# Kernel optimization log

Measured on AMD Instinct MI355X. Metric: run time of the kernel, lower is better.

Reference implementation:

```python
import jax, jax.numpy as jnp
import numpy as np

B, S, D = 2, 2048, 1024
H, KV, HD = 16, 4, 64
F, E, K = 2816, 8, 2
EPS = 1e-6

def setup_inputs() -> dict:
    key = jax.random.key(0)
    ks = jax.random.split(key, 9)
    def rn(k, shape, std=0.02):
        return jax.random.normal(k, shape, dtype=jnp.float32) * std
    inv_freq = 1.0 / (10000.0 ** (jnp.arange(0, HD, 2, dtype=jnp.float32) / HD))
    freqs = jnp.arange(S, dtype=jnp.float32)[:, None] * inv_freq[None, :]
    emb = jnp.concatenate([freqs, freqs], axis=-1)  # [S, HD]
    return {
        'hidden_states': rn(ks[0], (B, S, D), 1.0),
        'ln1_w': jnp.ones((D,), jnp.float32),
        'ln2_w': jnp.ones((D,), jnp.float32),
        'q_w': rn(ks[1], (H * HD, D)), 'q_b': jnp.zeros((H * HD,), jnp.float32),
        'k_w': rn(ks[2], (KV * HD, D)), 'k_b': jnp.zeros((KV * HD,), jnp.float32),
        'v_w': rn(ks[3], (KV * HD, D)), 'v_b': jnp.zeros((KV * HD,), jnp.float32),
        'o_w': rn(ks[4], (D, H * HD)),
        'router_w': rn(ks[5], (E, D), 0.01),
        'gate_w': rn(ks[6], (E, D, F)),
        'up_w': rn(ks[7], (E, D, F)),
        'down_w': rn(ks[8], (E, F, D)),
        'cos': jnp.cos(emb), 'sin': jnp.sin(emb),
    }

def _rmsnorm(x, w):
    v = jnp.mean(jnp.square(x.astype(jnp.float32)), axis=-1, keepdims=True)
    return (x.astype(jnp.float32) * jax.lax.rsqrt(v + EPS)).astype(x.dtype) * w

def _rotate_half(x):
    h = x.shape[-1] // 2
    return jnp.concatenate([-x[..., h:], x[..., :h]], axis=-1)

def reference(hidden_states, ln1_w, ln2_w, q_w, q_b, k_w, k_b, v_w, v_b, o_w, router_w, gate_w, up_w, down_w, cos, sin):
    # --- attention block (RMSNorm -> Qwen2Attention with RoPE+GQA -> residual) ---
    residual = hidden_states
    h = _rmsnorm(hidden_states, ln1_w)
    q = (h @ q_w.T + q_b).reshape(B, S, H, HD).transpose(0, 2, 1, 3)   # [B,H,S,HD]
    k = (h @ k_w.T + k_b).reshape(B, S, KV, HD).transpose(0, 2, 1, 3)  # [B,KV,S,HD]
    v = (h @ v_w.T + v_b).reshape(B, S, KV, HD).transpose(0, 2, 1, 3)
    c = cos[None, None]; s = sin[None, None]
    q = q * c + _rotate_half(q) * s
    k = k * c + _rotate_half(k) * s
    rep = H // KV
    k = jnp.repeat(k, rep, axis=1)
    v = jnp.repeat(v, rep, axis=1)
    scores = jnp.einsum('bhqd,bhkd->bhqk', q, k) / jnp.sqrt(jnp.float32(HD))
    causal = jnp.tril(jnp.ones((S, S), dtype=bool))
    scores = jnp.where(causal[None, None], scores, jnp.finfo(scores.dtype).min)
    attn = jax.nn.softmax(scores, axis=-1)
    ctx = jnp.einsum('bhqk,bhkd->bhqd', attn, v).transpose(0, 2, 1, 3).reshape(B, S, H * HD)
    x = ctx @ o_w.T + residual
    # --- MoE block (RMSNorm -> router -> expert SwiGLU MLPs -> combine -> residual) ---
    residual = x
    t = _rmsnorm(x, ln2_w).reshape(-1, D)  # [T, D], T = B*S
    logits = t @ router_w.T                # [T, E]
    probs = jax.nn.softmax(logits, axis=-1)
    topk_p, topk_i = jax.lax.top_k(probs, K)
    topk_p = topk_p / jnp.sum(topk_p, axis=-1, keepdims=True)
    # dispatch/combine weights [T,E]: vectorized form of the per-token scatter loop
    w = jnp.sum(jax.nn.one_hot(topk_i, E, dtype=t.dtype) * topk_p[..., None], axis=1)
    aux_loss = jnp.mean(E * jnp.square(jnp.mean(probs, axis=0)))
    out = jnp.zeros_like(t)
    for e in range(E):  # fixed small expert loop
        he = jax.nn.silu(t @ gate_w[e]) * (t @ up_w[e])
        out = out + (he @ down_w[e]) * w[:, e:e + 1]
    x = out.reshape(B, S, D) + residual
    return (x, aux_loss)
```

## Files before the change

kernel.cpp:

```cpp
#include <hip/hip_runtime.h>
#include <hip/hip_bf16.h>

#define DEVI __device__ __forceinline__

typedef float f32x4 __attribute__((ext_vector_type(4)));
typedef _Float16 f16x8 __attribute__((ext_vector_type(8)));
typedef short s16x8 __attribute__((ext_vector_type(8)));
typedef unsigned int u32;

constexpr int Bc = 2, Sc = 2048, Dc = 1024, Hc = 16, KVc = 4, HDc = 64, Fc = 2816, Ec = 8;
constexpr int Tc = Bc * Sc;
constexpr int QKVN = Hc * HDc + 2 * KVc * HDc;
constexpr int CAP = Tc * 2 + Ec * 128;
constexpr float LO_SCALE = 1024.0f;
constexpr float LO_INV = 1.0f / 1024.0f;

DEVI f32x4 mfma16(f16x8 a, f16x8 b, f32x4 c) {
    return __builtin_amdgcn_mfma_f32_16x16x32_f16(a, b, c, 0, 0, 0);
}
DEVI f32x4 mfma16(s16x8 a, s16x8 b, f32x4 c) {
    return __builtin_amdgcn_mfma_f32_16x16x32_bf16(a, b, c, 0, 0, 0);
}

DEVI void gll16(const void *g, void *l) {
    __builtin_amdgcn_global_load_lds(
        (const __attribute__((address_space(1))) u32 *)g,
        (__attribute__((address_space(3))) u32 *)l, 16, 0, 0);
}

DEVI u32 pack2(_Float16 a, _Float16 b) {
    union { _Float16 h[2]; u32 u; } t;
    t.h[0] = a; t.h[1] = b;
    return t.u;
}

template <int N> DEVI void wait_vm() {
    if constexpr (N == 0) asm volatile("s_waitcnt vmcnt(0)" ::: "memory");
    else if constexpr (N == 3) asm volatile("s_waitcnt vmcnt(3)" ::: "memory");
    else if constexpr (N == 4) asm volatile("s_waitcnt vmcnt(4)" ::: "memory");
    else if constexpr (N == 6) asm volatile("s_waitcnt vmcnt(6)" ::: "memory");
    else if constexpr (N == 8) asm volatile("s_waitcnt vmcnt(8)" ::: "memory");
}

template <typename VT> struct FragT;
template <> struct FragT<_Float16> { using type = f16x8; };
template <> struct FragT<__hip_bfloat16> { using type = s16x8; };

struct GemmP {
    const void *Ah, *Al;
    const void *Bh, *Bl, *Bh2;
    long lda, ldb, bExp, K;
    const int *poff, *gidx;
    const float *bias, *resid, *bw;
    float *outF, *outF2;
    __hip_bfloat16 *outBF;
    long ldc;
    int epi;
};

template <typename VT, bool SPLIT, bool GATHER, bool GU, int BN>
__global__ __launch_bounds__(256, SPLIT ? 3 : ((GU && BN == 128) ? 2 : 4)) void gemm_k(GemmP p) {
    constexpr int BM = 128;
    constexpr int NJ = BN / 32;
    constexpr bool HAS2 = SPLIT || GU;
    constexpr int ACH = SPLIT ? 1024 : 512;
    constexpr int BCH = BN * 4;
    constexpr int NB = HAS2 ? 2 : 1;
    constexpr int TOT = ACH + NB * BCH;
    constexpr int NCH = TOT / 256;
    constexpr int BUFVT = TOT * 8;
    constexpr int AOFF2 = 4096;
    constexpr int BOFF = ACH * 8;
    constexpr int B2OFF = (ACH + BCH) * 8;
    __shared__ __align__(16) VT s[2][BUFVT];
    const int tid = threadIdx.x, lane = tid & 63;
    const int wid = tid >> 6, wm = wid >> 1, wn = wid & 1;
    const int x = lane & 15, hi = lane >> 4;
    long m0 = (long)blockIdx.x * BM, n0 = (long)blockIdx.y * BN;
    int e = 0;
    if (p.poff) {
        int tot = p.poff[Ec];
        if (m0 >= tot) return;
        while (m0 >= p.poff[e + 1]) ++e;
    }

    const VT *gs[NCH];
    int chd[NCH];
#pragma unroll
    for (int i = 0; i < NCH; ++i) {
        int ch = tid + i * 256;
        chd[i] = ch;
        if (ch < ACH) {
            int slab = ch >> 9, local = ch & 511;
            int r = local >> 2, c = local & 3;
            int cs = c ^ ((r >> 1) & 3);
            long ar = m0 + r;
            if (GATHER) ar = p.gidx[ar];
            const VT *mat = (SPLIT && slab == 1) ? (const VT *)p.Al : (const VT *)p.Ah;
            gs[i] = mat + ar * p.lda + cs * 8;
        } else {
            int idx = ch - ACH;
            int which = idx / BCH, local = idx % BCH;
            int r = local >> 2, c = local & 3;
            int cs = c ^ ((r >> 1) & 3);
            const VT *bmat = (which == 0) ? (const VT *)p.Bh
                           : (SPLIT ? (const VT *)p.Bl : (const VT *)p.Bh2);
            gs[i] = bmat + (long)e * p.bExp + (n0 + r) * p.ldb + cs * 8;
        }
    }

    f32x4 acc[4][NJ];
    f32x4 acc2[HAS2 ? 4 : 1][HAS2 ? NJ : 1];
#pragma unroll
    for (int i = 0; i < 4; ++i)
#pragma unroll
        for (int j = 0; j < NJ; ++j) {
            acc[i][j] = (f32x4){0.f, 0.f, 0.f, 0.f};
            if constexpr (HAS2) acc2[i][j] = (f32x4){0.f, 0.f, 0.f, 0.f};
        }

    using F8 = typename FragT<VT>::type;
    const int KT = (int)(p.K / 32);
    auto stageTo = [&](int kt, int b) {
#pragma unroll
        for (int i = 0; i < NCH; ++i)
            gll16(gs[i] + (long)kt * 32, &s[b][(size_t)chd[i] * 8]);
    };

    stageTo(0, 0);
    if (KT > 1) stageTo(1, 1);

    for (int kt = 0; kt < KT; ++kt) {
        if (kt + 1 < KT) wait_vm<NCH>();
        else wait_vm<0>();
        __builtin_amdgcn_sched_barrier(0);
        __builtin_amdgcn_s_barrier();
        __builtin_amdgcn_sched_barrier(0);
        const int cur = kt & 1;

        F8 afh[4], afl[SPLIT ? 4 : 1];
#pragma unroll
        for (int mi = 0; mi < 4; ++mi) {
            int ar = wm * 64 + mi * 16 + x;
            int ad = (ar * 4 + (hi ^ ((ar >> 1) & 3))) * 8;
            afh[mi] = *(const F8 *)&s[cur][ad];
            if constexpr (SPLIT) afl[mi] = *(const F8 *)&s[cur][AOFF2 + ad];
        }
        __builtin_amdgcn_s_setprio(1);
#pragma unroll
        for (int nj = 0; nj < NJ; ++nj) {
            int br = wn * (BN / 2) + nj * 16 + x;
            int bd = (br * 4 + (hi ^ ((br >> 1) & 3))) * 8;
            F8 bfh = *(const F8 *)&s[cur][BOFF + bd];
            F8 bf2;
            if constexpr (HAS2) bf2 = *(const F8 *)&s[cur][B2OFF + bd];
#pragma unroll
            for (int mi = 0; mi < 4; ++mi) {
                acc[mi][nj] = mfma16(afh[mi], bfh, acc[mi][nj]);
                if constexpr (SPLIT) {
                    acc2[mi][nj] = mfma16(afh[mi], bf2, acc2[mi][nj]);
                    acc2[mi][nj] = mfma16(afl[mi], bfh, acc2[mi][nj]);
                }
                if constexpr (GU) acc2[mi][nj] = mfma16(afh[mi], bf2, acc2[mi][nj]);
            }
        }
        __builtin_amdgcn_s_setprio(0);

        asm volatile("s_waitcnt lgkmcnt(0)" ::: "memory");
        __builtin_amdgcn_sched_barrier(0);
        __builtin_amdgcn_s_barrier();
        __builtin_amdgcn_sched_barrier(0);
        if (kt + 2 < KT) stageTo(kt + 2, cur);
    }

#pragma unroll
    for (int mi = 0; mi < 4; ++mi)
#pragma unroll
        for (int nj = 0; nj < NJ; ++nj)
#pragma unroll
            for (int r = 0; r < 4; ++r) {
                long row = m0 + wm * 64 + mi * 16 + hi * 4 + r;
                long col = n0 + wn * (BN / 2) + nj * 16 + x;
                float v = acc[mi][nj][r];
                if constexpr (GU) {
                    float u = acc2[mi][nj][r];
                    float he = v / (1.f + __expf(-v)) * u;
                    p.outBF[row * p.ldc + col] = __float2bfloat16(he);
                } else {
                    if constexpr (SPLIT) v = fmaf(acc2[mi][nj][r], LO_INV, v);
                    switch (p.epi) {
                    case 0: p.outF[row * p.ldc + col] = v + p.bias[col]; break;
                    case 2: {
                        float o = v + p.resid[row * p.ldc + col];
                        p.outF[row * p.ldc + col] = o;
                        p.outF2[row * p.ldc + col] = o;
                    } break;
                    case 5: {
                        float wv = p.bw[row];
                        atomicAdd(&p.outF[(long)p.gidx[row] * p.ldc + col], v * wv);
                    } break;
                    }
                }
            }
}

__global__ __launch_bounds__(128, 2) void attn_k(
    const _Float16 *__restrict__ qh, const _Float16 *__restrict__ ql,
    const _Float16 *__restrict__ kh, const _Float16 *__restrict__ kl,
    const _Float16 *__restrict__ vTh, const _Float16 *__restrict__ vTl,
    _Float16 *__restrict__ ctxh, _Float16 *__restrict__ ctxl) {
    __shared__ __align__(16) _Float16 kbuf[2][2][32 * 64];
    __shared__ __align__(16) _Float16 vbuf[2][2][64 * 32];
    const int tid = threadIdx.x, lane = tid & 63, wid = tid >> 6;
    const int x = lane & 15, hi = lane >> 4;
    const int pairI = blockIdx.x;
    const int bh = blockIdx.y;
    const int b = bh >> 4, h = bh & 15, kvh = h >> 2;
    const long kRow0 = (long)b * Sc * 256;
    const long vRow0 = (long)(b * 4 + kvh) * 64 * (long)Sc;

    auto stage = [&](int kt, int bufI) {
        if (wid == 0) {
#pragma unroll
            for (int ss = 0; ss < 2; ++ss) {
                const _Float16 *src = ss ? kl : kh;
#pragma unroll
                for (int i = 0; i < 4; ++i) {
                    int kv = 8 * i + (lane >> 3);
                    int cd = (lane & 7) ^ (kv & 7);
                    const _Float16 *g = src + kRow0 + ((long)kt * 32 + kv) * 256 + kvh * 64 + cd * 8;
                    gll16(g, &kbuf[bufI][ss][i * 512]);
                }
            }
        } else {
#pragma unroll
            for (int ss = 0; ss < 2; ++ss) {
                const _Float16 *src = ss ? vTl : vTh;
#pragma unroll
                for (int i = 0; i < 4; ++i) {
                    int d = 16 * i + (lane >> 2);
                    int ckv = (lane & 3) ^ ((d >> 1) & 3);
                    const _Float16 *g = src + vRow0 + (long)d * Sc + (long)kt * 32 + ckv * 8;
                    gll16(g, &vbuf[bufI][ss][i * 512]);
                }
            }
        }
    };

    for (int seg = 0; seg < 2; ++seg) {
        const int qt = seg ? (63 - pairI) : pairI;
        const int q0 = qt * 32;
        const long qtokW = (long)b * Sc + q0 + wid * 16;

        f16x8 qfh[2], qfl[2];
#pragma unroll
        for (int ks = 0; ks < 2; ++ks) {
            long off = (qtokW + x) * (long)Dc + h * 64 + ks * 32 + hi * 8;
            qfh[ks] = *(const f16x8 *)(qh + off);
            qfl[ks] = *(const f16x8 *)(ql + off);
        }
        asm volatile("s_waitcnt vmcnt(0)" ::: "memory");
        __builtin_amdgcn_sched_barrier(0);

        f32x4 o1[4], o2[4];
        float mrow = -3.0e38f, lrow = 0.f;
#pragma unroll
        for (int dj = 0; dj < 4; ++dj) {
            o1[dj] = (f32x4){0.f, 0.f, 0.f, 0.f};
            o2[dj] = (f32x4){0.f, 0.f, 0.f, 0.f};
        }

        const int NT = qt + 1;

        stage(0, 0);
        stage(1, 1);

        for (int kt = 0; kt < NT; ++kt) {
            if (kt + 1 < NT) asm volatile("s_waitcnt vmcnt(8)" ::: "memory");
            else asm volatile("s_waitcnt vmcnt(0)" ::: "memory");
            __builtin_amdgcn_sched_barrier(0);
            __builtin_amdgcn_s_barrier();
            __builtin_amdgcn_sched_barrier(0);
            const int cur = kt & 1;

            f32x4 s1[2], s2[2];
#pragma unroll
            for (int kvs = 0; kvs < 2; ++kvs) {
                s1[kvs] = (f32x4){0.f, 0.f, 0.f, 0.f};
                s2[kvs] = (f32x4){0.f, 0.f, 0.f, 0.f};
            }
            __builtin_amdgcn_s_setprio(1);
#pragma unroll
            for (int ks = 0; ks < 2; ++ks)
#pragma unroll
                for (int kvs = 0; kvs < 2; ++kvs) {
                    int row = kvs * 16 + x;
                    int addr = row * 64 + (((ks * 4 + hi) ^ (row & 7)) << 3);
                    f16x8 kfh = *(const f16x8 *)&kbuf[cur][0][addr];
                    f16x8 kfl = *(const f16x8 *)&kbuf[cur][1][addr];
                    s1[kvs] = mfma16(kfh, qfh[ks], s1[kvs]);
                    s2[kvs] = mfma16(kfl, qfh[ks], s2[kvs]);
                    s2[kvs] = mfma16(kfh, qfl[ks], s2[kvs]);
                }
            __builtin_amdgcn_s_setprio(0);

            const bool diag = (kt == NT - 1);
            const int qpos = q0 + wid * 16 + x;
            float sv[2][4];
#pragma unroll
            for (int kvs = 0; kvs < 2; ++kvs)
#pragma unroll
                for (int r = 0; r < 4; ++r) {
                    float v = fmaf(s2[kvs][r], LO_INV, s1[kvs][r]) * 0.125f;
                    if (diag) {
                        int kvpos = kt * 32 + kvs * 16 + 4 * hi + r;
                        if (kvpos > qpos) v = -3.0e38f;
                    }
                    sv[kvs][r] = v;
                }
            float mx = sv[0][0];
#pragma unroll
            for (int kvs = 0; kvs < 2; ++kvs)
#pragma unroll
                for (int r = 0; r < 4; ++r) mx = fmaxf(mx, sv[kvs][r]);
            mx = fmaxf(mx, __shfl_xor(mx, 16));
            mx = fmaxf(mx, __shfl_xor(mx, 32));
            if (!__all(mx - mrow <= 8.0f)) {
                float mnew = fmaxf(mrow, mx);
                float scl = __expf(mrow - mnew);
                mrow = mnew;
                lrow *= scl;
                float sclr[4];
#pragma unroll
                for (int r = 0; r < 4; ++r) sclr[r] = __shfl(scl, 4 * hi + r);
#pragma unroll
                for (int dj = 0; dj < 4; ++dj)
#pragma unroll
                    for (int r = 0; r < 4; ++r) {
                        o1[dj][r] *= sclr[r];
                        o2[dj][r] *= sclr[r];
                    }
            }
            float pv[2][4];
            float ls = 0.f;
#pragma unroll
            for (int kvs = 0; kvs < 2; ++kvs)
#pragma unroll
                for (int r = 0; r < 4; ++r) {
                    pv[kvs][r] = __expf(sv[kvs][r] - mrow);
                    ls += pv[kvs][r];
                }
            ls += __shfl_xor(ls, 16);
            ls += __shfl_xor(ls, 32);
            lrow += ls;
            u32 Bh0[2], Bh1[2], Bl0[2], Bl1[2];
#pragma unroll
            for (int pr = 0; pr < 2; ++pr) {
                _Float16 a0 = (_Float16)pv[0][2 * pr], a1 = (_Float16)pv[0][2 * pr + 1];
                _Float16 b0 = (_Float16)pv[1][2 * pr], b1 = (_Float16)pv[1][2 * pr + 1];
                Bh0[pr] = pack2(a0, a1);
                Bh1[pr] = pack2(b0, b1);
                _Float16 la0 = (_Float16)((pv[0][2 * pr] - (float)a0) * LO_SCALE);
                _Float16 la1 = (_Float16)((pv[0][2 * pr + 1] - (float)a1) * LO_SCALE);
                _Float16 lb0 = (_Float16)((pv[1][2 * pr] - (float)b0) * LO_SCALE);
                _Float16 lb1 = (_Float16)((pv[1][2 * pr + 1] - (float)b1) * LO_SCALE);
                Bl0[pr] = pack2(la0, la1);
                Bl1[pr] = pack2(lb0, lb1);
            }
            const int srcLow = x + ((lane & 16) ? 32 : 0);
            const int srcHigh = srcLow + 16;
            const bool useB1 = lane >= 32;
            union { u32 u[4]; f16x8 v; } fh, fl;
#pragma unroll
            for (int pr = 0; pr < 2; ++pr) {
                u32 t0 = (u32)__shfl((int)Bh0[pr], srcLow);
                u32 t1 = (u32)__shfl((int)Bh1[pr], srcLow);
                fh.u[pr] = useB1 ? t1 : t0;
                u32 u0 = (u32)__shfl((int)Bh0[pr], srcHigh);
                u32 u1 = (u32)__shfl((int)Bh1[pr], srcHigh);
                fh.u[2 + pr] = useB1 ? u1 : u0;
                u32 s0 = (u32)__shfl((int)Bl0[pr], srcLow);
                u32 s1v = (u32)__shfl((int)Bl1[pr], srcLow);
                fl.u[pr] = useB1 ? s1v : s0;
                u32 w0 = (u32)__shfl((int)Bl0[pr], srcHigh);
                u32 w1 = (u32)__shfl((int)Bl1[pr], srcHigh);
                fl.u[2 + pr] = useB1 ? w1 : w0;
            }
            f16x8 pah = fh.v, pal = fl.v;

            __builtin_amdgcn_s_setprio(1);
#pragma unroll
            for (int dj = 0; dj < 4; ++dj) {
                int d = dj * 16 + x;
                int addr = d * 32 + ((hi ^ ((d >> 1) & 3)) << 3);
                f16x8 vhf = *(const f16x8 *)&vbuf[cur][0][addr];
                f16x8 vlf = *(const f16x8 *)&vbuf[cur][1][addr];
                o1[dj] = mfma16(pah, vhf, o1[dj]);
                o2[dj] = mfma16(pah, vlf, o2[dj]);
                o2[dj] = mfma16(pal, vhf, o2[dj]);
            }
            __builtin_amdgcn_s_setprio(0);

            asm volatile("s_waitcnt lgkmcnt(0)" ::: "memory");
            __builtin_amdgcn_sched_barrier(0);
            __builtin_amdgcn_s_barrier();
            __builtin_amdgcn_sched_barrier(0);
            if (kt + 2 < NT) stage(kt + 2, cur);
        }

        float linv = 1.0f / lrow;
        float lr[4];
#pragma unroll
        for (int r = 0; r < 4; ++r) lr[r] = __shfl(linv, 4 * hi + r);
#pragma unroll
        for (int dj = 0; dj < 4; ++dj)
#pragma unroll
            for (int r = 0; r < 4; ++r) {
                long tok = qtokW + 4 * hi + r;
                float ov = fmaf(o2[dj][r], LO_INV, o1[dj][r]) * lr[r];
                _Float16 hv = (_Float16)ov;
                long off = tok * Dc + h * 64 + dj * 16 + x;
                ctxh[off] = hv;
                ctxl[off] = (_Float16)((ov - (float)hv) * LO_SCALE);
            }
    }
}

__global__ __launch_bounds__(256) void rmsnorm_split_k(const float *__restrict__ x,
        const float *__restrict__ w, _Float16 *__restrict__ oh, _Float16 *__restrict__ ol) {
    const long row = blockIdx.x;
    const int tid = threadIdx.x, lane = tid & 63, wid = tid >> 6;
    f32x4 v = *(const f32x4 *)(x + row * Dc + tid * 4);
    float ss = v[0] * v[0] + v[1] * v[1] + v[2] * v[2] + v[3] * v[3];
#pragma unroll
    for (int off = 1; off < 64; off <<= 1) ss += __shfl_xor(ss, off);
    __shared__ float sw[4];
    if (lane == 0) sw[wid] = ss;
    __syncthreads();
    float inv = 1.0f / sqrtf((sw[0] + sw[1] + sw[2] + sw[3]) * (1.f / Dc) + 1e-6f);
#pragma unroll
    for (int j = 0; j < 4; ++j) {
        float y = v[j] * inv * w[tid * 4 + j];
        _Float16 hv = (_Float16)y;
        oh[row * Dc + tid * 4 + j] = hv;
        ol[row * Dc + tid * 4 + j] = (_Float16)((y - (float)hv) * LO_SCALE);
    }
}

__global__ __launch_bounds__(256) void rmsnorm2_k(const float *__restrict__ x,
        const float *__restrict__ w, float *__restrict__ tf, __hip_bfloat16 *__restrict__ tb) {
    const long row = blockIdx.x;
    const int tid = threadIdx.x, lane = tid & 63, wid = tid >> 6;
    f32x4 v = *(const f32x4 *)(x + row * Dc + tid * 4);
    float ss = v[0] * v[0] + v[1] * v[1] + v[2] * v[2] + v[3] * v[3];
#pragma unroll
    for (int off = 1; off < 64; off <<= 1) ss += __shfl_xor(ss, off);
    __shared__ float sw[4];
    if (lane == 0) sw[wid] = ss;
    __syncthreads();
    float inv = 1.0f / sqrtf((sw[0] + sw[1] + sw[2] + sw[3]) * (1.f / Dc) + 1e-6f);
#pragma unroll
    for (int j = 0; j < 4; ++j) {
        float y = v[j] * inv * w[tid * 4 + j];
        tf[row * Dc + tid * 4 + j] = y;
        tb[row * Dc + tid * 4 + j] = __float2bfloat16(y);
    }
}

__global__ void split_f16_k(const float *__restrict__ x, _Float16 *hi, _Float16 *lo, long n) {
    for (long i = (long)blockIdx.x * 256 + threadIdx.x; i < n; i += (long)gridDim.x * 256) {
        float v = x[i];
        _Float16 h = (_Float16)v;
        hi[i] = h;
        lo[i] = (_Float16)((v - (float)h) * LO_SCALE);
    }
}

__global__ void pack_qkvw_k(const float *__restrict__ qw, const float *__restrict__ kw,
        const float *__restrict__ vw, _Float16 *wh, _Float16 *wl) {
    const long n = (long)QKVN * Dc;
    for (long i = (long)blockIdx.x * 256 + threadIdx.x; i < n; i += (long)gridDim.x * 256) {
        long o = i >> 10;
        int d = (int)(i & 1023);
        float v;
        if (o < 1024) v = qw[o * 1024 + d];
        else if (o < 1280) v = kw[(o - 1024) * 1024 + d];
        else v = vw[(o - 1280) * 1024 + d];
        _Float16 h = (_Float16)v;
        wh[i] = h;
        wl[i] = (_Float16)((v - (float)h) * LO_SCALE);
    }
}

__global__ void pack_bias_k(const float *qb, const float *kb, const float *vb, float *out) {
    int i = blockIdx.x * 256 + threadIdx.x;
    if (i >= QKVN) return;
    out[i] = (i < 1024) ? qb[i] : (i < 1280) ? kb[i - 1024] : vb[i - 1280];
}

__global__ __launch_bounds__(256) void transpose_bf16_k(const float *__restrict__ in,
        __hip_bfloat16 *__restrict__ out, int R, int C) {
    __shared__ float tile[64 * 65];
    const long eo = (long)blockIdx.z * R * C;
    const int r0 = blockIdx.y * 64, c0 = blockIdx.x * 64;
#pragma unroll
    for (int i = 0; i < 16; ++i) {
        int idx = threadIdx.x + i * 256;
        int r = idx >> 6, c = idx & 63;
        tile[r * 65 + c] = in[eo + (long)(r0 + r) * C + (c0 + c)];
    }
    __syncthreads();
#pragma unroll
    for (int i = 0; i < 16; ++i) {
        int idx = threadIdx.x + i * 256;
        int cc = idx >> 6, rr = idx & 63;
        out[eo + (long)(c0 + cc) * R + (r0 + rr)] = __float2bfloat16(tile[rr * 65 + cc]);
    }
}

__global__ __launch_bounds__(256) void vtrans_k(const float *__restrict__ qkvf,
        _Float16 *__restrict__ vTh, _Float16 *__restrict__ vTl) {
    __shared__ float tile[64][65];
    const int tok0 = blockIdx.x * 64;
    const int bk = blockIdx.y;
    const int b = bk >> 2, kvh = bk & 3;
#pragma unroll
    for (int it = 0; it < 16; ++it) {
        int idx = it * 256 + threadIdx.x;
        int r = idx >> 6, c = idx & 63;
        tile[r][c] = qkvf[((long)b * Sc + tok0 + r) * QKVN + 1280 + kvh * 64 + c];
    }
    __syncthreads();
    const int d = threadIdx.x & 63, ch = threadIdx.x >> 6;
    long orow = ((long)bk * 64 + d) * (long)Sc + tok0 + ch * 16;
    f16x8 oh[2], ol[2];
#pragma unroll
    for (int j = 0; j < 16; ++j) {
        float v = tile[ch * 16 + j][d];
        _Float16 hv = (_Float16)v;
        oh[j >> 3][j & 7] = hv;
        ol[j >> 3][j & 7] = (_Float16)((v - (float)hv) * LO_SCALE);
    }
    *(f16x8 *)(vTh + orow) = oh[0];
    *(f16x8 *)(vTh + orow + 8) = oh[1];
    *(f16x8 *)(vTl + orow) = ol[0];
    *(f16x8 *)(vTl + orow + 8) = ol[1];
}

__global__ __launch_bounds__(256) void rope_k(const float *__restrict__ qkv,
        const float *__restrict__ cosb, const float *__restrict__ sinb,
        _Float16 *qh, _Float16 *ql, _Float16 *kh2, _Float16 *kl2) {
    const long tok = blockIdx.x;
    const int s = (int)(tok % Sc);
    const float *row = qkv + tok * QKVN;
    for (int p = threadIdx.x; p < 640; p += 256) {
        int u = p >> 5, d = p & 31;
        float x1 = row[u * 64 + d], x2 = row[u * 64 + d + 32];
        float cs = cosb[(long)s * 64 + d], sn = sinb[(long)s * 64 + d];
        float o1v = x1 * cs - x2 * sn;
        float o2v = x2 * cs + x1 * sn;
        _Float16 h1 = (_Float16)o1v, h2 = (_Float16)o2v;
        _Float16 l1 = (_Float16)((o1v - (float)h1) * LO_SCALE);
        _Float16 l2 = (_Float16)((o2v - (float)h2) * LO_SCALE);
        if (u < 16) {
            long off = tok * 1024 + u * 64 + d;
            qh[off] = h1; ql[off] = l1; qh[off + 32] = h2; ql[off + 32] = l2;
        } else {
            long off = tok * 256 + (u - 16) * 64 + d;
            kh2[off] = h1; kl2[off] = l1; kh2[off + 32] = h2; kl2[off + 32] = l2;
        }
    }
}

__global__ __launch_bounds__(256) void router_p1_k(const float *__restrict__ t,
        const float *__restrict__ rw, float *probs, int *tok_e, float *tok_w, int *cnt) {
    const int tid = threadIdx.x, lane = tid & 63, wid = tid >> 6;
    const long tok = (long)blockIdx.x * 4 + wid;
    const float *row = t + tok * Dc;
    const int d0 = lane * 16;
    f32x4 xv[4];
#pragma unroll
    for (int i = 0; i < 4; ++i) xv[i] = *(const f32x4 *)(row + d0 + i * 4);
    float acc[8];
#pragma unroll
    for (int e = 0; e < 8; ++e) {
        const float *wr = rw + (long)e * Dc + d0;
        float a = 0.f;
#pragma unroll
        for (int i = 0; i < 4; ++i) {
            f32x4 wv = *(const f32x4 *)(wr + i * 4);
            a += xv[i][0] * wv[0] + xv[i][1] * wv[1] + xv[i][2] * wv[2] + xv[i][3] * wv[3];
        }
        acc[e] = a;
    }
#pragma unroll
    for (int off = 1; off < 64; off <<= 1)
#pragma unroll
        for (int e = 0; e < 8; ++e) acc[e] += __shfl_xor(acc[e], off);
    if (lane == 0) {
        float mx = acc[0];
#pragma unroll
        for (int e = 1; e < 8; ++e) mx = fmaxf(mx, acc[e]);
        float ex[8], s = 0.f;
#pragma unroll
        for (int e = 0; e < 8; ++e) { ex[e] = expf(acc[e] - mx); s += ex[e]; }
        float inv = 1.f / s;
        int i1 = -1, i2 = -1;
        float p1v = -1.f, p2v = -1.f;
#pragma unroll
        for (int e = 0; e < 8; ++e) {
            float pe = ex[e] * inv;
            probs[tok * 8 + e] = pe;
            if (pe > p1v) { i2 = i1; p2v = p1v; i1 = e; p1v = pe; }
            else if (pe > p2v) { i2 = e; p2v = pe; }
        }
        float wsum = p1v + p2v;
        tok_e[tok * 2] = i1; tok_e[tok * 2 + 1] = i2;
        tok_w[tok * 2] = p1v / wsum; tok_w[tok * 2 + 1] = p2v / wsum;
        atomicAdd(&cnt[i1], 1);
        atomicAdd(&cnt[i2], 1);
    }
}

__global__ __launch_bounds__(1024) void router_p2_k(const int *cnt, const float *probs,
        int *poff, float *aux_out) {
    __shared__ float sd[1024];
    const int tid = threadIdx.x;
    const int e = tid & 7, rs = tid >> 3;
    float s = 0.f;
    for (int r = rs; r < Tc; r += 128) s += probs[(long)r * 8 + e];
    sd[tid] = s;
    __syncthreads();
    for (int st = 64; st >= 1; st >>= 1) {
        if (rs < st) sd[tid] += sd[tid + st * 8];
        __syncthreads();
    }
    if (tid == 0) {
        float a = 0.f;
        for (int ee = 0; ee < 8; ++ee) {
            float m = sd[ee] * (1.f / Tc);
            a += m * m;
        }
        aux_out[0] = a;
        int o = 0;
        poff[0] = 0;
        for (int ee = 0; ee < 8; ++ee) { o += (cnt[ee] + 127) & ~127; poff[ee + 1] = o; }
    }
}

__global__ void router_p3_k(const int *tok_e, const float *tok_w, const int *poff,
        int *cursor, int *btok, float *bw) {
    long tok = (long)blockIdx.x * 256 + threadIdx.x;
    if (tok >= Tc) return;
#pragma unroll
    for (int j = 0; j < 2; ++j) {
        int e = tok_e[tok * 2 + j];
        int slot = atomicAdd(&cursor[e], 1);
        btok[poff[e] + slot] = (int)tok;
        bw[poff[e] + slot] = tok_w[tok * 2 + j];
    }
}

__global__ void router_p4_k(const int *poff, const int *cnt, int *btok, float *bw) {
    int s = blockIdx.x * 256 + threadIdx.x;
    if (s >= poff[8]) return;
    int e = 0;
    while (s >= poff[e + 1]) ++e;
    if (s - poff[e] >= cnt[e]) { btok[s] = 0; bw[s] = 0.f; }
}

extern "C" void kernel_launch(void *const *d_in, const int *in_sizes, int n_in,
                              void *d_out, int out_size, void *d_ws, size_t ws_size,
                              hipStream_t stream) {
    (void)in_sizes; (void)n_in;
    const float *hidden = (const float *)d_in[0];
    const float *ln1 = (const float *)d_in[1];
    const float *ln2 = (const float *)d_in[2];
    const float *qw = (const float *)d_in[3];
    const float *qb = (const float *)d_in[4];
    const float *kw = (const float *)d_in[5];
    const float *kb = (const float *)d_in[6];
    const float *vw = (const float *)d_in[7];
    const float *vb = (const float *)d_in[8];
    const float *ow = (const float *)d_in[9];
    const float *rw = (const float *)d_in[10];
    const float *gw = (const float *)d_in[11];
    const float *uw = (const float *)d_in[12];
    const float *dwn = (const float *)d_in[13];
    const float *cosb = (const float *)d_in[14];
    const float *sinb = (const float *)d_in[15];
    float *outx = (float *)d_out;

    char *base = (char *)d_ws;
    size_t off = 0;
    auto alloc = [&](size_t bytes) -> char * {
        char *p = base + off;
        off += (bytes + 255) & ~(size_t)255;
        return p;
    };
    _Float16 *qkvwh = (_Float16 *)alloc((size_t)QKVN * Dc * 2);
    _Float16 *qkvwl = (_Float16 *)alloc((size_t)QKVN * Dc * 2);
    float *qkvb = (float *)alloc(QKVN * 4);
    _Float16 *owh = (_Float16 *)alloc((size_t)Dc * Dc * 2);
    _Float16 *owl = (_Float16 *)alloc((size_t)Dc * Dc * 2);
    __hip_bfloat16 *gateT = (__hip_bfloat16 *)alloc((size_t)Ec * Fc * Dc * 2);
    __hip_bfloat16 *upT = (__hip_bfloat16 *)alloc((size_t)Ec * Fc * Dc * 2);
    __hip_bfloat16 *downT = (__hip_bfloat16 *)alloc((size_t)Ec * Dc * Fc * 2);
    char *U2 = alloc((size_t)Tc * Dc * 4);
    _Float16 *hh = (_Float16 *)U2;
    _Float16 *hl = hh + (size_t)Tc * Dc;
    float *tf = (float *)U2;
    char *U3 = alloc((size_t)Tc * Dc * 4);
    _Float16 *qhb = (_Float16 *)U3;
    _Float16 *qlb = qhb + (size_t)Tc * Dc;
    float *x1 = (float *)U3;
    _Float16 *khb = (_Float16 *)alloc((size_t)Tc * 256 * 2);
    _Float16 *klb = (_Float16 *)alloc((size_t)Tc * 256 * 2);
    _Float16 *vTh = (_Float16 *)alloc((size_t)Tc * 256 * 2);
    _Float16 *vTl = (_Float16 *)alloc((size_t)Tc * 256 * 2);
    _Float16 *ctxh = (_Float16 *)alloc((size_t)Tc * Dc * 2);
    _Float16 *ctxl = (_Float16 *)alloc((size_t)Tc * Dc * 2);
    __hip_bfloat16 *tbf = (__hip_bfloat16 *)alloc((size_t)Tc * Dc * 2);
    float *probs = (float *)alloc((size_t)Tc * 8 * 4);
    int *tok_e = (int *)alloc((size_t)Tc * 2 * 4);
    float *tok_w = (float *)alloc((size_t)Tc * 2 * 4);
    int *cnt = (int *)alloc(256);
    int *cursor = cnt + 8;
    int *poff = (int *)alloc(256);
    int *btok = (int *)alloc((size_t)CAP * 4);
    float *bwgt = (float *)alloc((size_t)CAP * 4);
    size_t qkvfB = (size_t)Tc * QKVN * 4;
    size_t gbufB = (size_t)CAP * Fc * 2;
    size_t u1B = qkvfB > gbufB ? qkvfB : gbufB;
    char *U1 = alloc(u1B);
    float *qkvf = (float *)U1;
    __hip_bfloat16 *gbuf = (__hip_bfloat16 *)U1;

    if (off > ws_size) {
        hipMemsetAsync(d_out, 0, (size_t)out_size * 4, stream);
        return;
    }

    hipMemsetAsync(cnt, 0, 64, stream);
    pack_qkvw_k<<<1024, 256, 0, stream>>>(qw, kw, vw, qkvwh, qkvwl);
    pack_bias_k<<<(QKVN + 255) / 256, 256, 0, stream>>>(qb, kb, vb, qkvb);
    split_f16_k<<<1024, 256, 0, stream>>>(ow, owh, owl, (long)Dc * Dc);
    transpose_bf16_k<<<dim3(Fc / 64, Dc / 64, Ec), 256, 0, stream>>>(gw, gateT, Dc, Fc);
    transpose_bf16_k<<<dim3(Fc / 64, Dc / 64, Ec), 256, 0, stream>>>(uw, upT, Dc, Fc);
    transpose_bf16_k<<<dim3(Dc / 64, Fc / 64, Ec), 256, 0, stream>>>(dwn, downT, Fc, Dc);
    rmsnorm_split_k<<<Tc, 256, 0, stream>>>(hidden, ln1, hh, hl);

    GemmP g{};
    g.Ah = hh; g.Al = hl; g.Bh = qkvwh; g.Bl = qkvwl;
    g.lda = Dc; g.ldb = Dc; g.bExp = 0; g.K = Dc;
    g.bias = qkvb; g.outF = qkvf; g.ldc = QKVN; g.epi = 0;
    gemm_k<_Float16, true, false, false, 64><<<dim3(Tc / 128, QKVN / 64), 256, 0, stream>>>(g);

    rope_k<<<Tc, 256, 0, stream>>>(qkvf, cosb, sinb, qhb, qlb, khb, klb);
    vtrans_k<<<dim3(Sc / 64, Bc * KVc), 256, 0, stream>>>(qkvf, vTh, vTl);
    attn_k<<<dim3(Sc / 64, Bc * Hc), 128, 0, stream>>>(qhb, qlb, khb, klb, vTh, vTl, ctxh, ctxl);

    GemmP go{};
    go.Ah = ctxh; go.Al = ctxl; go.Bh = owh; go.Bl = owl;
    go.lda = Dc; go.ldb = Dc; go.bExp = 0; go.K = Dc;
    go.resid = hidden; go.outF = x1; go.outF2 = outx; go.ldc = Dc; go.epi = 2;
    gemm_k<_Float16, true, false, false, 64><<<dim3(Tc / 128, Dc / 64), 256, 0, stream>>>(go);

    rmsnorm2_k<<<Tc, 256, 0, stream>>>(x1, ln2, tf, tbf);
    router_p1_k<<<Tc / 4, 256, 0, stream>>>(tf, rw, probs, tok_e, tok_w, cnt);
    router_p2_k<<<1, 1024, 0, stream>>>(cnt, probs, poff, outx + (long)Tc * Dc);
    router_p3_k<<<Tc / 256, 256, 0, stream>>>(tok_e, tok_w, poff, cursor, btok, bwgt);
    router_p4_k<<<CAP / 256, 256, 0, stream>>>(poff, cnt, btok, bwgt);

    GemmP gg{};
    gg.Ah = tbf; gg.Bh = gateT; gg.Bh2 = upT;
    gg.lda = Dc; gg.ldb = Dc; gg.bExp = (long)Fc * Dc; gg.K = Dc;
    gg.poff = poff; gg.gidx = btok; gg.outBF = gbuf; gg.ldc = Fc;
    gemm_k<__hip_bfloat16, false, true, true, 128><<<dim3(CAP / 128, Fc / 128), 256, 0, stream>>>(gg);

    GemmP gd{};
    gd.Ah = gbuf; gd.Bh = downT;
    gd.lda = Fc; gd.ldb = Fc; gd.bExp = (long)Dc * Fc; gd.K = Fc;
    gd.poff = poff; gd.gidx = btok; gd.bw = bwgt;
    gd.outF = outx; gd.ldc = Dc; gd.epi = 5;
    gemm_k<__hip_bfloat16, false, false, false, 64><<<dim3(CAP / 128, Dc / 64), 256, 0, stream>>>(gd);
}
```

Measured before the change: 801.2 us.

## Replace atomic scatter in down-proj with slot buffer and combine kernel

```diff
diff --git a/kernel.cpp b/kernel.cpp
--- a/kernel.cpp
+++ b/kernel.cpp
@@ -195,13 +195,25 @@
                         p.outF[row * p.ldc + col] = o;
                         p.outF2[row * p.ldc + col] = o;
                     } break;
-                    case 5: {
-                        float wv = p.bw[row];
-                        atomicAdd(&p.outF[(long)p.gidx[row] * p.ldc + col], v * wv);
-                    } break;
+                    case 5:
+                        p.outF[row * p.ldc + col] = v * p.bw[row];
+                        break;
                     }
                 }
             }
+}
+
+__global__ __launch_bounds__(256) void combine_k(const float *__restrict__ scat,
+        const int *__restrict__ tok_slot, float *__restrict__ out) {
+    const long tok = blockIdx.x;
+    const int c = threadIdx.x * 4;
+    const long s0 = tok_slot[tok * 2], s1 = tok_slot[tok * 2 + 1];
+    f32x4 a = *(const f32x4 *)(scat + s0 * Dc + c);
+    f32x4 b = *(const f32x4 *)(scat + s1 * Dc + c);
+    f32x4 o = *(const f32x4 *)(out + tok * Dc + c);
+#pragma unroll
+    for (int j = 0; j < 4; ++j) o[j] += a[j] + b[j];
+    *(f32x4 *)(out + tok * Dc + c) = o;
 }
 
 __global__ __launch_bounds__(128, 2) void attn_k(
@@ -649,7 +661,7 @@
 }
 
 __global__ void router_p3_k(const int *tok_e, const float *tok_w, const int *poff,
-        int *cursor, int *btok, float *bw) {
+        int *cursor, int *btok, float *bw, int *tok_slot) {
     long tok = (long)blockIdx.x * 256 + threadIdx.x;
     if (tok >= Tc) return;
 #pragma unroll
@@ -658,6 +670,7 @@
         int slot = atomicAdd(&cursor[e], 1);
         btok[poff[e] + slot] = (int)tok;
         bw[poff[e] + slot] = tok_w[tok * 2 + j];
+        tok_slot[tok * 2 + j] = poff[e] + slot;
     }
 }
 
@@ -718,12 +731,14 @@
     _Float16 *klb = (_Float16 *)alloc((size_t)Tc * 256 * 2);
     _Float16 *vTh = (_Float16 *)alloc((size_t)Tc * 256 * 2);
     _Float16 *vTl = (_Float16 *)alloc((size_t)Tc * 256 * 2);
+    float *scat = (float *)U2;
     _Float16 *ctxh = (_Float16 *)alloc((size_t)Tc * Dc * 2);
     _Float16 *ctxl = (_Float16 *)alloc((size_t)Tc * Dc * 2);
     __hip_bfloat16 *tbf = (__hip_bfloat16 *)alloc((size_t)Tc * Dc * 2);
     float *probs = (float *)alloc((size_t)Tc * 8 * 4);
     int *tok_e = (int *)alloc((size_t)Tc * 2 * 4);
     float *tok_w = (float *)alloc((size_t)Tc * 2 * 4);
+    int *tok_slot = (int *)alloc((size_t)Tc * 2 * 4);
     int *cnt = (int *)alloc(256);
     int *cursor = cnt + 8;
     int *poff = (int *)alloc(256);
@@ -769,7 +784,7 @@
     rmsnorm2_k<<<Tc, 256, 0, stream>>>(x1, ln2, tf, tbf);
     router_p1_k<<<Tc / 4, 256, 0, stream>>>(tf, rw, probs, tok_e, tok_w, cnt);
     router_p2_k<<<1, 1024, 0, stream>>>(cnt, probs, poff, outx + (long)Tc * Dc);
-    router_p3_k<<<Tc / 256, 256, 0, stream>>>(tok_e, tok_w, poff, cursor, btok, bwgt);
+    router_p3_k<<<Tc / 256, 256, 0, stream>>>(tok_e, tok_w, poff, cursor, btok, bwgt, tok_slot);
     router_p4_k<<<CAP / 256, 256, 0, stream>>>(poff, cnt, btok, bwgt);
 
     GemmP gg{};
@@ -781,7 +796,9 @@
     GemmP gd{};
     gd.Ah = gbuf; gd.Bh = downT;
     gd.lda = Fc; gd.ldb = Fc; gd.bExp = (long)Dc * Fc; gd.K = Fc;
-    gd.poff = poff; gd.gidx = btok; gd.bw = bwgt;
-    gd.outF = outx; gd.ldc = Dc; gd.epi = 5;
-    gemm_k<__hip_bfloat16, false, false, false, 64><<<dim3(CAP / 128, Dc / 64), 256, 0, stream>>>(gd);
-}
+    gd.poff = poff; gd.bw = bwgt;
+    gd.outF = scat; gd.ldc = Dc; gd.epi = 5;
+    gemm_k<__hip_bfloat16, false, false, false, 128><<<dim3(CAP / 128, Dc / 128), 256, 0, stream>>>(gd);
+
+    combine_k<<<Tc, 256, 0, stream>>>(scat, tok_slot, outx);
+}
```

Result: faster. 745.5 us (-6.9%).
